# Optimization experiments

Measured on AMD Instinct MI355X. Metric: run time of the kernel, lower is better.

Reference implementation:

```python
import jax, jax.numpy as jnp
import numpy as np

N_NODES = 50000
N_EDGES = 800000
DIM = 128
LN_EPS = 1e-5


def setup_inputs() -> dict:
    key = jax.random.key(0)
    k1, k2, k3, k4, k5 = jax.random.split(key, 5)
    x = jax.random.normal(k1, (N_NODES, DIM), dtype=jnp.float32)
    edge_index = jax.random.randint(k2, (2, N_EDGES), 0, N_NODES, dtype=jnp.int64)
    edge_weight = jax.random.uniform(k3, (N_EDGES,), dtype=jnp.float32)
    # GCNConv linear (PyG Linear: out = x @ W.T + b)
    W = jax.random.normal(k4, (DIM, DIM), dtype=jnp.float32) / np.sqrt(DIM)
    b = jnp.zeros((DIM,), dtype=jnp.float32)
    # pygnn.LayerNorm(dim, mode='node') affine params
    ln_weight = jnp.ones((DIM,), dtype=jnp.float32)
    ln_bias = jnp.zeros((DIM,), dtype=jnp.float32)
    return {"x": x, "edge_index": edge_index, "edge_weight": edge_weight,
            "W": W, "b": b, "ln_weight": ln_weight, "ln_bias": ln_bias}


def reference(x, edge_index, edge_weight, W, b, ln_weight, ln_bias):
    n = x.shape[0]
    # --- LayerNorm (mode='node'): per-node over feature dim ---
    mu = jnp.mean(x, axis=-1, keepdims=True)
    var = jnp.mean(jnp.square(x - mu), axis=-1, keepdims=True)
    xn = (x - mu) * jax.lax.rsqrt(var + LN_EPS) * ln_weight + ln_bias
    # --- GCNConv: linear first, then normalized propagate ---
    h = xn @ W.T  # [N, dim]
    row, col = edge_index[0], edge_index[1]  # source, target
    # add self loops (fill_value = 1.0)
    loop = jnp.arange(n, dtype=edge_index.dtype)
    row_f = jnp.concatenate([row, loop])
    col_f = jnp.concatenate([col, loop])
    ew_f = jnp.concatenate([edge_weight, jnp.ones((n,), dtype=edge_weight.dtype)])
    # symmetric gcn normalization: deg over target (col)
    deg = jax.ops.segment_sum(ew_f, col_f, num_segments=n)
    dinv = jnp.where(deg > 0, jax.lax.rsqrt(deg), 0.0)
    norm = dinv[row_f] * ew_f * dinv[col_f]  # [E+N]
    # gather-scale-scatter
    msg = h[row_f] * norm[:, None]  # [E+N, dim]
    out = jax.ops.segment_sum(msg, col_f, num_segments=n) + b
    # --- GELU (torch default = exact erf form); dropout is identity (p=0 / eval) ---
    return jax.nn.gelu(out, approximate=False)
```

## Files before the change

### kernel.cpp

```cpp
#include <hip/hip_runtime.h>
#include <math.h>

#define DIM 128
#define LN_EPS 1e-5f
#define TWO32 4294967296.0
#define INV32 (1.0 / 4294967296.0)

typedef __attribute__((ext_vector_type(8))) short short8;
typedef __attribute__((ext_vector_type(4))) float floatx4;

__device__ __forceinline__ float gelu_exact(float v) {
    return 0.5f * v * (1.0f + erff(v * 0.70710678118654752f));
}
__device__ __forceinline__ float bf2f(unsigned short u) {
    return __uint_as_float(((unsigned)u) << 16);
}
__device__ __forceinline__ short f2bf(float f) {
    unsigned b = __float_as_uint(f);
    return (short)((b + 0x7FFF + ((b >> 16) & 1)) >> 16);
}

__global__ __launch_bounds__(256) void gemm_rank_kernel(
    const float* __restrict__ x, const float* __restrict__ W,
    const float* __restrict__ lnw, const float* __restrict__ lnb,
    unsigned short* __restrict__ h16,
    const int* __restrict__ col, const float* __restrict__ ew,
    double* __restrict__ acc8, int* __restrict__ rnk,
    int n, int E)
{
    const int tid = threadIdx.x;

    if ((int)(blockIdx.x % 3) == 2) {
        int rb   = blockIdx.x / 3;
        int r    = rb & 7;
        size_t rbase = (size_t)r * n;
        int base = rb * 2048 + tid;
        #pragma unroll
        for (int it = 0; it < 8; ++it) {
            int e = base + it * 256;
            if (e < E) {
                int c = col[e];
                double old = atomicAdd(&acc8[rbase + c], TWO32 + (double)ew[e]);
                int rk = (int)(old * INV32);
                rnk[e] = (r << 24) | rk;
            }
        }
        return;
    }

    __shared__ short swb[2048 * 8];
    __shared__ short axb[1024 * 8];

    const int gb = blockIdx.x - (blockIdx.x + 1) / 3;
    const int n0 = gb * 64;

    for (int c = tid; c < 2048; c += 256) {
        int nrow = ((c >> 8) << 4) | (c & 15);
        int kb   = (((c >> 6) & 3) << 5) + (((c >> 4) & 3) << 3);
        const float* wp = W + nrow * DIM + kb;
        float4 w0 = *(const float4*)wp;
        float4 w1 = *(const float4*)(wp + 4);
        short8 p;
        p[0] = f2bf(w0.x); p[1] = f2bf(w0.y); p[2] = f2bf(w0.z); p[3] = f2bf(w0.w);
        p[4] = f2bf(w1.x); p[5] = f2bf(w1.y); p[6] = f2bf(w1.z); p[7] = f2bf(w1.w);
        *(short8*)&swb[c * 8] = p;
    }

    {
        int m = tid >> 2, sub = tid & 3;
        int node = n0 + m;
        bool valid = (node < n);
        const float4* xp = (const float4*)(x + (size_t)node * DIM + sub * 32);
        float4 v[8];
        float s = 0.f, ss = 0.f;
        #pragma unroll
        for (int i = 0; i < 8; ++i) {
            v[i] = valid ? xp[i] : make_float4(0.f, 0.f, 0.f, 0.f);
            s  += v[i].x + v[i].y + v[i].z + v[i].w;
            ss += v[i].x * v[i].x + v[i].y * v[i].y + v[i].z * v[i].z + v[i].w * v[i].w;
        }
        s += __shfl_xor(s, 1); ss += __shfl_xor(ss, 1);
        s += __shfl_xor(s, 2); ss += __shfl_xor(ss, 2);
        float mu   = s * (1.0f / 128.0f);
        float var  = ss * (1.0f / 128.0f) - mu * mu;
        float rstd = rsqrtf(var + LN_EPS);

        int mt = m >> 4, mloc = m & 15;
        #pragma unroll
        for (int quad = 0; quad < 4; ++quad) {
            float4 a = v[2 * quad], c4 = v[2 * quad + 1];
            const float4* lw = (const float4*)(lnw + sub * 32 + quad * 8);
            const float4* lb = (const float4*)(lnb + sub * 32 + quad * 8);
            float4 lw0 = lw[0], lw1 = lw[1], lb0 = lb[0], lb1 = lb[1];
            short8 p;
            p[0] = f2bf((a.x  - mu) * rstd * lw0.x + lb0.x);
            p[1] = f2bf((a.y  - mu) * rstd * lw0.y + lb0.y);
            p[2] = f2bf((a.z  - mu) * rstd * lw0.z + lb0.z);
            p[3] = f2bf((a.w  - mu) * rstd * lw0.w + lb0.w);
            p[4] = f2bf((c4.x - mu) * rstd * lw1.x + lb1.x);
            p[5] = f2bf((c4.y - mu) * rstd * lw1.y + lb1.y);
            p[6] = f2bf((c4.z - mu) * rstd * lw1.z + lb1.z);
            p[7] = f2bf((c4.w - mu) * rstd * lw1.w + lb1.w);
            int slot = mt * 256 + sub * 64 + quad * 16 + mloc;
            *(short8*)&axb[slot * 8] = p;
        }
    }
    __syncthreads();

    const int w    = tid >> 6;
    const int lane = tid & 63;

    short8 afrag[4];
    #pragma unroll
    for (int kq = 0; kq < 4; ++kq)
        afrag[kq] = *(const short8*)&axb[(w * 256 + kq * 64 + lane) * 8];

    floatx4 acc[8];
    #pragma unroll
    for (int jt = 0; jt < 8; ++jt) acc[jt] = (floatx4){0.f, 0.f, 0.f, 0.f};

    #pragma unroll
    for (int jt = 0; jt < 8; ++jt) {
        #pragma unroll
        for (int kq = 0; kq < 4; ++kq) {
            short8 bfrag = *(const short8*)&swb[(jt * 256 + kq * 64 + lane) * 8];
            acc[jt] = __builtin_amdgcn_mfma_f32_16x16x32_bf16(afrag[kq], bfrag,
                                                              acc[jt], 0, 0, 0);
        }
    }

    const int quad = lane >> 4, nl = lane & 15;
    #pragma unroll
    for (int jt = 0; jt < 8; ++jt) {
        #pragma unroll
        for (int r = 0; r < 4; ++r) {
            int rnode = n0 + w * 16 + quad * 4 + r;
            if (rnode < n)
                h16[(size_t)rnode * DIM + jt * 16 + nl] = (unsigned short)f2bf(acc[jt][r]);
        }
    }
}

__global__ __launch_bounds__(256) void scan_a_kernel(
    const double* __restrict__ acc8, int* __restrict__ bsum, int n)
{
    __shared__ int lds[256];
    int t = threadIdx.x, b = blockIdx.x;
    int base = b * 1024 + t * 4;
    int s = 0;
    #pragma unroll
    for (int i = 0; i < 4; ++i) {
        int c = base + i;
        if (c < n) {
            int k = 0;
            for (int r = 0; r < 8; ++r)
                k += (int)(acc8[(size_t)r * n + c] * INV32);
            s += k;
        }
    }
    lds[t] = s; __syncthreads();
    for (int off = 128; off > 0; off >>= 1) {
        if (t < off) lds[t] += lds[t + off];
        __syncthreads();
    }
    if (t == 0) bsum[b] = lds[0];
}

__global__ __launch_bounds__(256) void scan_bc_kernel(
    const double* __restrict__ acc8, const int* __restrict__ bsum,
    int* __restrict__ off8, float* __restrict__ dinv, int nb, int n)
{
    __shared__ int lds[256];
    int t = threadIdx.x, b = blockIdx.x;
    int pre0 = 0, total = 0;
    for (int i = 0; i < nb; ++i) {
        int v = bsum[i];
        if (i < b) pre0 += v;
        total += v;
    }
    int base = b * 1024 + t * 4;

    int k8[4][8];
    int ksum[4];
    double wsum[4];
    #pragma unroll
    for (int i = 0; i < 4; ++i) {
        ksum[i] = 0; wsum[i] = 0.0;
        int c = base + i;
        if (c < n) {
            for (int r = 0; r < 8; ++r) {
                double v = acc8[(size_t)r * n + c];
                int k = (int)(v * INV32);
                k8[i][r] = k;
                ksum[i] += k;
                wsum[i] += v - (double)k * TWO32;
            }
        }
    }
    int s = ksum[0] + ksum[1] + ksum[2] + ksum[3];
    lds[t] = s; __syncthreads();
    int inc = s;
    for (int off = 1; off < 256; off <<= 1) {
        int add = (t >= off) ? lds[t - off] : 0;
        __syncthreads();
        inc += add;
        lds[t] = inc;
        __syncthreads();
    }
    int pre = pre0 + inc - s;
    #pragma unroll
    for (int i = 0; i < 4; ++i) {
        int c = base + i;
        if (c < n) {
            int run = pre;
            for (int r = 0; r < 8; ++r) {
                off8[(size_t)r * (n + 1) + c] = run;
                run += k8[i][r];
            }
            dinv[c] = rsqrtf(1.0f + (float)wsum[i]);
            pre = run;
        }
    }
    if (b == 0 && t == 0) off8[n] = total;
}

__global__ __launch_bounds__(256) void scatter_fill_kernel(
    const int* __restrict__ row, const int* __restrict__ col,
    const float* __restrict__ ew, const int* __restrict__ rnk,
    const int* __restrict__ off8, const float* __restrict__ dinv,
    int2* __restrict__ edge_s, int n, int E)
{
    int e = blockIdx.x * 256 + threadIdx.x;
    if (e < E) {
        int c  = col[e];
        int pk = rnk[e];
        int r  = pk >> 24;
        int rk = pk & 0xFFFFFF;
        int pos = off8[(size_t)r * (n + 1) + c] + rk;
        int src = row[e];
        float nr = dinv[src] * ew[e] * dinv[c];
        edge_s[pos] = make_int2(src, __float_as_int(nr));
    }
}

__global__ __launch_bounds__(256) void gather4_kernel(
    const int* __restrict__ offsets, const int2* __restrict__ edge_s,
    const float* __restrict__ dinv, const unsigned short* __restrict__ h16,
    const float* __restrict__ bias, float* __restrict__ out, int n)
{
    int wave = (blockIdx.x * 256 + threadIdx.x) >> 6;
    int lane = threadIdx.x & 63;
    int grp  = lane >> 4;
    int sub  = lane & 15;
    int node = wave * 4 + grp;
    if (node >= n) return;

    int beg = offsets[node], end = offsets[node + 1];
    float di = dinv[node];
    short8 sv = *(const short8*)(h16 + (size_t)node * DIM + sub * 8);
    float s2 = di * di;
    float acc[8];
    #pragma unroll
    for (int d = 0; d < 8; ++d) acc[d] = s2 * bf2f((unsigned short)sv[d]);

    int j = beg;
    for (; j + 3 < end; j += 4) {
        int2 e0 = edge_s[j],     e1 = edge_s[j + 1];
        int2 e2 = edge_s[j + 2], e3 = edge_s[j + 3];
        short8 a0 = *(const short8*)(h16 + (size_t)e0.x * DIM + sub * 8);
        short8 a1 = *(const short8*)(h16 + (size_t)e1.x * DIM + sub * 8);
        short8 a2 = *(const short8*)(h16 + (size_t)e2.x * DIM + sub * 8);
        short8 a3 = *(const short8*)(h16 + (size_t)e3.x * DIM + sub * 8);
        float n0 = __int_as_float(e0.y), n1 = __int_as_float(e1.y);
        float n2 = __int_as_float(e2.y), n3 = __int_as_float(e3.y);
        #pragma unroll
        for (int d = 0; d < 8; ++d) {
            acc[d] = fmaf(n0, bf2f((unsigned short)a0[d]), acc[d]);
            acc[d] = fmaf(n1, bf2f((unsigned short)a1[d]), acc[d]);
            acc[d] = fmaf(n2, bf2f((unsigned short)a2[d]), acc[d]);
            acc[d] = fmaf(n3, bf2f((unsigned short)a3[d]), acc[d]);
        }
    }
    for (; j < end; ++j) {
        int2 e0 = edge_s[j];
        float n0 = __int_as_float(e0.y);
        short8 a = *(const short8*)(h16 + (size_t)e0.x * DIM + sub * 8);
        #pragma unroll
        for (int d = 0; d < 8; ++d) acc[d] = fmaf(n0, bf2f((unsigned short)a[d]), acc[d]);
    }

    float4 b0 = *(const float4*)(bias + sub * 8);
    float4 b1 = *(const float4*)(bias + sub * 8 + 4);
    float4 o0, o1;
    o0.x = gelu_exact(acc[0] + b0.x); o0.y = gelu_exact(acc[1] + b0.y);
    o0.z = gelu_exact(acc[2] + b0.z); o0.w = gelu_exact(acc[3] + b0.w);
    o1.x = gelu_exact(acc[4] + b1.x); o1.y = gelu_exact(acc[5] + b1.y);
    o1.z = gelu_exact(acc[6] + b1.z); o1.w = gelu_exact(acc[7] + b1.w);
    float* op = out + (size_t)node * DIM + sub * 8;
    *(float4*)op       = o0;
    *(float4*)(op + 4) = o1;
}

extern "C" void kernel_launch(void* const* d_in, const int* in_sizes, int n_in,
                              void* d_out, int out_size, void* d_ws, size_t ws_size,
                              hipStream_t stream)
{
    const float* x    = (const float*)d_in[0];
    const int*   ei   = (const int*)d_in[1];
    const float* ew   = (const float*)d_in[2];
    const float* W    = (const float*)d_in[3];
    const float* b    = (const float*)d_in[4];
    const float* ln_w = (const float*)d_in[5];
    const float* ln_b = (const float*)d_in[6];
    float* out = (float*)d_out;

    const int n = in_sizes[0] / DIM;
    const int E = in_sizes[2];
    const int* row  = ei;
    const int* colp = ei + E;

    const int NB = (n + 1023) / 1024;

    double*         acc8    = (double*)d_ws;
    int2*           edge_s  = (int2*)(acc8 + (size_t)8 * n);
    unsigned short* h16     = (unsigned short*)(edge_s + E);
    int*            rnk     = (int*)(h16 + (size_t)n * DIM);
    int*            off8    = rnk + E;
    int*            bsum    = off8 + (size_t)8 * (n + 1);
    float*          dinv    = (float*)(bsum + 4096);

    const int GB = (n + 63) / 64;
    const int RB = (E + 2047) / 2048;
    int T = GB + RB;
    while (T / 3 < RB || T - T / 3 < GB) ++T;

    hipMemsetAsync(acc8, 0, (size_t)8 * n * sizeof(double), stream);
    gemm_rank_kernel<<<T, 256, 0, stream>>>(x, W, ln_w, ln_b, h16,
                                            colp, ew, acc8, rnk, n, E);
    scan_a_kernel<<<NB, 256, 0, stream>>>(acc8, bsum, n);
    scan_bc_kernel<<<NB, 256, 0, stream>>>(acc8, bsum, off8, dinv, NB, n);
    scatter_fill_kernel<<<(E + 255) / 256, 256, 0, stream>>>(row, colp, ew, rnk,
                                                             off8, dinv, edge_s, n, E);
    {
        int waves  = (n + 3) / 4;
        int blocks = (waves + 3) / 4;
        gather4_kernel<<<blocks, 256, 0, stream>>>(off8, edge_s, dinv, h16, b, out, n);
    }
}
```

Before: 193.8 us.

## Replace global double-atomic CSR build with two-level bucket sort via LDS histograms

Replaces the global fp64 atomic counting and rank scheme with a two-pass bucket sort. LDS histograms over 64-node buckets per edge chunk are built alongside the GEMM, followed by a column scan, an LDS-atomic bucket scatter, and a per-bucket CSR pass that also computes degrees and dinv. The per-edge normalization moves into the gather kernel as an extra dinv lookup. This removes the memset and contended global atomics, but adds an extra pass over the edges and packs the source index into 16 bits, which only holds while node count is at most 65536.

```diff
diff --git a/kernel.cpp b/kernel.cpp
--- a/kernel.cpp
+++ b/kernel.cpp
@@ -3,8 +3,7 @@
 
 #define DIM 128
 #define LN_EPS 1e-5f
-#define TWO32 4294967296.0
-#define INV32 (1.0 / 4294967296.0)
+#define HB 256
 
 typedef __attribute__((ext_vector_type(8))) short short8;
 typedef __attribute__((ext_vector_type(4))) float floatx4;
@@ -20,38 +19,34 @@
     return (short)((b + 0x7FFF + ((b >> 16) & 1)) >> 16);
 }
 
-__global__ __launch_bounds__(256) void gemm_rank_kernel(
+__global__ __launch_bounds__(256) void gemm_hist_kernel(
     const float* __restrict__ x, const float* __restrict__ W,
     const float* __restrict__ lnw, const float* __restrict__ lnb,
     unsigned short* __restrict__ h16,
-    const int* __restrict__ col, const float* __restrict__ ew,
-    double* __restrict__ acc8, int* __restrict__ rnk,
-    int n, int E)
-{
-    const int tid = threadIdx.x;
-
-    if ((int)(blockIdx.x % 3) == 2) {
-        int rb   = blockIdx.x / 3;
-        int r    = rb & 7;
-        size_t rbase = (size_t)r * n;
-        int base = rb * 2048 + tid;
-        #pragma unroll
-        for (int it = 0; it < 8; ++it) {
-            int e = base + it * 256;
-            if (e < E) {
-                int c = col[e];
-                double old = atomicAdd(&acc8[rbase + c], TWO32 + (double)ew[e]);
-                int rk = (int)(old * INV32);
-                rnk[e] = (r << 24) | rk;
-            }
-        }
-        return;
-    }
-
+    const int* __restrict__ col, int* __restrict__ hist,
+    int n, int E, int nbkt)
+{
     __shared__ short swb[2048 * 8];
     __shared__ short axb[1024 * 8];
-
-    const int gb = blockIdx.x - (blockIdx.x + 1) / 3;
+    const int tid = threadIdx.x;
+
+    if ((int)blockIdx.x < HB) {
+        int* lh = (int*)swb;
+        for (int b = tid; b < nbkt; b += 256) lh[b] = 0;
+        __syncthreads();
+        int g = blockIdx.x;
+        int chunk = (E + HB - 1) / HB;
+        int e0 = g * chunk;
+        int e1 = e0 + chunk; if (e1 > E) e1 = E;
+        for (int e = e0 + tid; e < e1; e += 256)
+            atomicAdd(&lh[col[e] >> 6], 1);
+        __syncthreads();
+        for (int b = tid; b < nbkt; b += 256)
+            hist[(size_t)g * nbkt + b] = lh[b];
+        return;
+    }
+
+    const int gb = blockIdx.x - HB;
     const int n0 = gb * 64;
 
     for (int c = tid; c < 2048; c += 256) {
@@ -141,105 +136,130 @@
     }
 }
 
-__global__ __launch_bounds__(256) void scan_a_kernel(
-    const double* __restrict__ acc8, int* __restrict__ bsum, int n)
-{
-    __shared__ int lds[256];
-    int t = threadIdx.x, b = blockIdx.x;
-    int base = b * 1024 + t * 4;
-    int s = 0;
-    #pragma unroll
-    for (int i = 0; i < 4; ++i) {
-        int c = base + i;
-        if (c < n) {
-            int k = 0;
-            for (int r = 0; r < 8; ++r)
-                k += (int)(acc8[(size_t)r * n + c] * INV32);
-            s += k;
-        }
-    }
-    lds[t] = s; __syncthreads();
-    for (int off = 128; off > 0; off >>= 1) {
-        if (t < off) lds[t] += lds[t + off];
+__global__ __launch_bounds__(256) void scan_kernel(
+    const int* __restrict__ hist, int* __restrict__ base,
+    int* __restrict__ bktbase, int E, int nbkt)
+{
+    __shared__ int ls[256];
+    const int tid = threadIdx.x;
+    const int nq  = (nbkt + 255) / 256;
+
+    int sums[4];
+    #pragma unroll
+    for (int q = 0; q < 4; ++q) {
+        int b = q * 256 + tid;
+        int s = 0;
+        if (q < nq && b < nbkt) {
+            const int* hp = hist + b;
+            for (int g = 0; g < HB; g += 4) {
+                s += hp[(size_t)g * nbkt] + hp[(size_t)(g + 1) * nbkt]
+                   + hp[(size_t)(g + 2) * nbkt] + hp[(size_t)(g + 3) * nbkt];
+            }
+        }
+        sums[q] = s;
+    }
+
+    int excl[4];
+    int carry = 0;
+    #pragma unroll
+    for (int q = 0; q < 4; ++q) {
+        int v = sums[q];
         __syncthreads();
-    }
-    if (t == 0) bsum[b] = lds[0];
-}
-
-__global__ __launch_bounds__(256) void scan_bc_kernel(
-    const double* __restrict__ acc8, const int* __restrict__ bsum,
-    int* __restrict__ off8, float* __restrict__ dinv, int nb, int n)
-{
-    __shared__ int lds[256];
-    int t = threadIdx.x, b = blockIdx.x;
-    int pre0 = 0, total = 0;
-    for (int i = 0; i < nb; ++i) {
-        int v = bsum[i];
-        if (i < b) pre0 += v;
-        total += v;
-    }
-    int base = b * 1024 + t * 4;
-
-    int k8[4][8];
-    int ksum[4];
-    double wsum[4];
-    #pragma unroll
-    for (int i = 0; i < 4; ++i) {
-        ksum[i] = 0; wsum[i] = 0.0;
-        int c = base + i;
-        if (c < n) {
-            for (int r = 0; r < 8; ++r) {
-                double v = acc8[(size_t)r * n + c];
-                int k = (int)(v * INV32);
-                k8[i][r] = k;
-                ksum[i] += k;
-                wsum[i] += v - (double)k * TWO32;
-            }
-        }
-    }
-    int s = ksum[0] + ksum[1] + ksum[2] + ksum[3];
-    lds[t] = s; __syncthreads();
-    int inc = s;
-    for (int off = 1; off < 256; off <<= 1) {
-        int add = (t >= off) ? lds[t - off] : 0;
+        ls[tid] = v;
         __syncthreads();
-        inc += add;
-        lds[t] = inc;
-        __syncthreads();
-    }
-    int pre = pre0 + inc - s;
-    #pragma unroll
-    for (int i = 0; i < 4; ++i) {
-        int c = base + i;
-        if (c < n) {
-            int run = pre;
-            for (int r = 0; r < 8; ++r) {
-                off8[(size_t)r * (n + 1) + c] = run;
-                run += k8[i][r];
-            }
-            dinv[c] = rsqrtf(1.0f + (float)wsum[i]);
-            pre = run;
-        }
-    }
-    if (b == 0 && t == 0) off8[n] = total;
-}
-
-__global__ __launch_bounds__(256) void scatter_fill_kernel(
+        int inc = v;
+        for (int off = 1; off < 256; off <<= 1) {
+            int add = (tid >= off) ? ls[tid - off] : 0;
+            __syncthreads();
+            inc += add;
+            ls[tid] = inc;
+            __syncthreads();
+        }
+        excl[q] = carry + inc - v;
+        carry += ls[255];
+    }
+
+    if (blockIdx.x == 0) {
+        #pragma unroll
+        for (int q = 0; q < 4; ++q) {
+            int b = q * 256 + tid;
+            if (b < nbkt) bktbase[b] = excl[q];
+        }
+        if (tid == 0) bktbase[nbkt] = E;
+    }
+
+    int q = blockIdx.x;
+    int b = q * 256 + tid;
+    if (b < nbkt) {
+        int run = excl[q];
+        for (int g = 0; g < HB; ++g) {
+            size_t idx = (size_t)g * nbkt + b;
+            int v = hist[idx];
+            base[idx] = run;
+            run += v;
+        }
+    }
+}
+
+__global__ __launch_bounds__(256) void bucket_scatter_kernel(
     const int* __restrict__ row, const int* __restrict__ col,
-    const float* __restrict__ ew, const int* __restrict__ rnk,
-    const int* __restrict__ off8, const float* __restrict__ dinv,
-    int2* __restrict__ edge_s, int n, int E)
-{
-    int e = blockIdx.x * 256 + threadIdx.x;
-    if (e < E) {
-        int c  = col[e];
-        int pk = rnk[e];
-        int r  = pk >> 24;
-        int rk = pk & 0xFFFFFF;
-        int pos = off8[(size_t)r * (n + 1) + c] + rk;
-        int src = row[e];
-        float nr = dinv[src] * ew[e] * dinv[c];
-        edge_s[pos] = make_int2(src, __float_as_int(nr));
+    const float* __restrict__ ew, const int* __restrict__ base,
+    int2* __restrict__ srt, int E, int nbkt)
+{
+    __shared__ int cur[1024];
+    const int tid = threadIdx.x, g = blockIdx.x;
+    for (int b = tid; b < nbkt; b += 256)
+        cur[b] = base[(size_t)g * nbkt + b];
+    __syncthreads();
+    int chunk = (E + HB - 1) / HB;
+    int e0 = g * chunk;
+    int e1 = e0 + chunk; if (e1 > E) e1 = E;
+    for (int e = e0 + tid; e < e1; e += 256) {
+        int c = col[e];
+        int pos = atomicAdd(&cur[c >> 6], 1);
+        srt[pos] = make_int2(((c & 63) << 16) | row[e], __float_as_int(ew[e]));
+    }
+}
+
+__global__ __launch_bounds__(256) void csr_kernel(
+    const int2* __restrict__ srt, const int* __restrict__ bktbase,
+    int2* __restrict__ edge_s, int* __restrict__ offsets,
+    float* __restrict__ dinv, int n, int E)
+{
+    __shared__ int   k64[64];
+    __shared__ float w64[64];
+    __shared__ int   off64[64];
+    __shared__ int   cur64[64];
+    const int tid = threadIdx.x, b = blockIdx.x;
+    if (tid < 64) { k64[tid] = 0; w64[tid] = 0.f; }
+    __syncthreads();
+    int s0 = bktbase[b], s1 = bktbase[b + 1];
+    for (int i = s0 + tid; i < s1; i += 256) {
+        int2 v = srt[i];
+        int d = (v.x >> 16) & 63;
+        atomicAdd(&k64[d], 1);
+        atomicAdd(&w64[d], __int_as_float(v.y));
+    }
+    __syncthreads();
+    if (tid == 0) {
+        int run = 0;
+        #pragma unroll
+        for (int d = 0; d < 64; ++d) { off64[d] = run; cur64[d] = run; run += k64[d]; }
+    }
+    __syncthreads();
+    if (tid < 64) {
+        int dest = b * 64 + tid;
+        if (dest < n) {
+            offsets[dest] = s0 + off64[tid];
+            dinv[dest]    = rsqrtf(1.0f + w64[tid]);
+        }
+    }
+    if (b == 0 && tid == 0) offsets[n] = E;
+    for (int i = s0 + tid; i < s1; i += 256) {
+        int2 v = srt[i];
+        int d = (v.x >> 16) & 63;
+        int p = atomicAdd(&cur64[d], 1);
+        edge_s[s0 + p] = make_int2(v.x & 0xFFFF, v.y);
     }
 }
 
@@ -271,8 +291,10 @@
         short8 a1 = *(const short8*)(h16 + (size_t)e1.x * DIM + sub * 8);
         short8 a2 = *(const short8*)(h16 + (size_t)e2.x * DIM + sub * 8);
         short8 a3 = *(const short8*)(h16 + (size_t)e3.x * DIM + sub * 8);
-        float n0 = __int_as_float(e0.y), n1 = __int_as_float(e1.y);
-        float n2 = __int_as_float(e2.y), n3 = __int_as_float(e3.y);
+        float n0 = dinv[e0.x] * __int_as_float(e0.y) * di;
+        float n1 = dinv[e1.x] * __int_as_float(e1.y) * di;
+        float n2 = dinv[e2.x] * __int_as_float(e2.y) * di;
+        float n3 = dinv[e3.x] * __int_as_float(e3.y) * di;
         #pragma unroll
         for (int d = 0; d < 8; ++d) {
             acc[d] = fmaf(n0, bf2f((unsigned short)a0[d]), acc[d]);
@@ -283,7 +305,7 @@
     }
     for (; j < end; ++j) {
         int2 e0 = edge_s[j];
-        float n0 = __int_as_float(e0.y);
+        float n0 = dinv[e0.x] * __int_as_float(e0.y) * di;
         short8 a = *(const short8*)(h16 + (size_t)e0.x * DIM + sub * 8);
         #pragma unroll
         for (int d = 0; d < 8; ++d) acc[d] = fmaf(n0, bf2f((unsigned short)a[d]), acc[d]);
@@ -318,32 +340,27 @@
     const int E = in_sizes[2];
     const int* row  = ei;
     const int* colp = ei + E;
-
-    const int NB = (n + 1023) / 1024;
-
-    double*         acc8    = (double*)d_ws;
-    int2*           edge_s  = (int2*)(acc8 + (size_t)8 * n);
+    const int nbkt = (n + 63) / 64;
+
+    int2*           srt     = (int2*)d_ws;
+    int2*           edge_s  = srt + E;
     unsigned short* h16     = (unsigned short*)(edge_s + E);
-    int*            rnk     = (int*)(h16 + (size_t)n * DIM);
-    int*            off8    = rnk + E;
-    int*            bsum    = off8 + (size_t)8 * (n + 1);
-    float*          dinv    = (float*)(bsum + 4096);
+    int*            hist    = (int*)(h16 + (size_t)n * DIM);
+    int*            base    = hist + (size_t)HB * nbkt;
+    int*            bktbase = base + (size_t)HB * nbkt;
+    int*            offsets = bktbase + nbkt + 1;
+    float*          dinv    = (float*)(offsets + n + 1);
 
     const int GB = (n + 63) / 64;
-    const int RB = (E + 2047) / 2048;
-    int T = GB + RB;
-    while (T / 3 < RB || T - T / 3 < GB) ++T;
-
-    hipMemsetAsync(acc8, 0, (size_t)8 * n * sizeof(double), stream);
-    gemm_rank_kernel<<<T, 256, 0, stream>>>(x, W, ln_w, ln_b, h16,
-                                            colp, ew, acc8, rnk, n, E);
-    scan_a_kernel<<<NB, 256, 0, stream>>>(acc8, bsum, n);
-    scan_bc_kernel<<<NB, 256, 0, stream>>>(acc8, bsum, off8, dinv, NB, n);
-    scatter_fill_kernel<<<(E + 255) / 256, 256, 0, stream>>>(row, colp, ew, rnk,
-                                                             off8, dinv, edge_s, n, E);
+
+    gemm_hist_kernel<<<HB + GB, 256, 0, stream>>>(x, W, ln_w, ln_b, h16,
+                                                  colp, hist, n, E, nbkt);
+    scan_kernel<<<(nbkt + 255) / 256, 256, 0, stream>>>(hist, base, bktbase, E, nbkt);
+    bucket_scatter_kernel<<<HB, 256, 0, stream>>>(row, colp, ew, base, srt, E, nbkt);
+    csr_kernel<<<nbkt, 256, 0, stream>>>(srt, bktbase, edge_s, offsets, dinv, n, E);
     {
         int waves  = (n + 3) / 4;
         int blocks = (waves + 3) / 4;
-        gather4_kernel<<<blocks, 256, 0, stream>>>(off8, edge_s, dinv, h16, b, out, n);
-    }
-}
+        gather4_kernel<<<blocks, 256, 0, stream>>>(offsets, edge_s, dinv, h16, b, out, n);
+    }
+}
```

Result: slower. 228.2 us (+17.8%).
